# Kernel optimization log

Hardware: AMD Instinct MI355X
Metric: run time of the kernel (lower is better)

Reference implementation:

```python
import jax, jax.numpy as jnp
import numpy as np

K_PLG = 9
LN_EPS = 1e-5

def _layer_norm(x, g, b):
    mu = jnp.mean(x, axis=-1, keepdims=True)
    v = jnp.mean((x - mu) ** 2, axis=-1, keepdims=True)
    return (x - mu) / jnp.sqrt(v + LN_EPS) * g + b

def _label_to_patch_agg(label, patch, k):
    # squared euclidean distances (S, N); sqrt is monotonic so top-k indices
    # match torch.cdist(p=2).topk(largest=False)
    d2 = (jnp.sum(label * label, axis=1)[:, None]
          + jnp.sum(patch * patch, axis=1)[None, :]
          - 2.0 * label @ patch.T)
    _, idx = jax.lax.top_k(-d2, k)          # (S, k) nearest
    nbr = patch[idx]                         # (S, k, C)
    return jnp.max(nbr - label[:, None, :], axis=1)  # max-relative diff (S, C)

def setup_inputs() -> dict:
    key = jax.random.key(0)
    ks = jax.random.split(key, 12)
    N, C = 100000, 256
    n_mood, n_genre, n_sub = 64, 256, 1024
    s = 1.0 / np.sqrt(C)
    return {
        "patch_emb": jax.random.normal(ks[0], (N, C), jnp.float32),
        "mood_emb": jax.random.normal(ks[1], (n_mood, C), jnp.float32),
        "genre_emb": jax.random.normal(ks[2], (n_genre, C), jnp.float32),
        "sub_emb": jax.random.normal(ks[3], (n_sub, C), jnp.float32),
        "Wm": jax.random.normal(ks[4], (2 * C, C), jnp.float32) * s,
        "bm": jnp.zeros((C,), jnp.float32),
        "Wg": jax.random.normal(ks[5], (3 * C, C), jnp.float32) * s,
        "bg": jnp.zeros((C,), jnp.float32),
        "Ws": jax.random.normal(ks[6], (4 * C, C), jnp.float32) * s,
        "bs": jnp.zeros((C,), jnp.float32),
        "gm": jnp.ones((C,), jnp.float32), "bnm": jnp.zeros((C,), jnp.float32),
        "gg": jnp.ones((C,), jnp.float32), "bng": jnp.zeros((C,), jnp.float32),
        "gs": jnp.ones((C,), jnp.float32), "bns": jnp.zeros((C,), jnp.float32),
    }

def reference(patch_emb, mood_emb, genre_emb, sub_emb,
              Wm, bm, Wg, bg, Ws, bs, gm, bnm, gg, bng, gs, bns):
    k = K_PLG
    # mood level
    ctx_m = _label_to_patch_agg(mood_emb, patch_emb, k)
    mood = _layer_norm(
        mood_emb + jnp.concatenate([mood_emb, ctx_m], axis=-1) @ Wm + bm, gm, bnm)
    # genre level
    ctx_g_p = _label_to_patch_agg(genre_emb, patch_emb, k)
    ctx_g_m = _label_to_patch_agg(genre_emb, mood, max(1, k // 2))
    genre = _layer_norm(
        genre_emb + jnp.concatenate([genre_emb, ctx_g_p, ctx_g_m], axis=-1) @ Wg + bg,
        gg, bng)
    # sub-genre level
    ctx_s_p = _label_to_patch_agg(sub_emb, patch_emb, k)
    ctx_s_m = _label_to_patch_agg(sub_emb, mood, max(1, k // 3))
    ctx_s_g = _label_to_patch_agg(sub_emb, genre, max(1, k // 2))
    sub = _layer_norm(
        sub_emb + jnp.concatenate([sub_emb, ctx_s_p, ctx_s_m, ctx_s_g], axis=-1) @ Ws + bs,
        gs, bns)
    return (mood, genre, sub)
```

## Files before the change

### kernel.cpp

```cpp
#include <hip/hip_runtime.h>
#include <float.h>

#define N_PATCH 100000
#define C 256
#define S_TOT 1344
#define LBLK 32
#define NGRP 42
#define NCHUNK 24
#define CHUNKP 4224
#define NTILE 1563
#define KCC 10
#define NCAND (NCHUNK*KCC)
#define NSEL 24
#define KP 9
#define SMASK 0xFFFFE000u
#define KINIT 0x7F7FFFFFu

typedef __attribute__((ext_vector_type(4))) float f32x4;
typedef __attribute__((ext_vector_type(2))) long i64x2;
typedef __attribute__((ext_vector_type(4))) unsigned int u32x4;

static __device__ __forceinline__ unsigned int pk4_fp8(float a, float b, float c, float d) {
  int v = __builtin_amdgcn_cvt_pk_fp8_f32(a, b, 0, false);
  v = __builtin_amdgcn_cvt_pk_fp8_f32(c, d, v, true);
  return (unsigned int)v;
}

#define KNET3(K0, K1, K2, KV)                               \
  { unsigned int _kv = (KV);                                \
    K2 = min(K2, max(K1, _kv));                             \
    K1 = min(K1, max(K0, _kv));                             \
    K0 = min(K0, _kv); }

__global__ __launch_bounds__(256) void k_prep(
    const float* __restrict__ patch, const float* __restrict__ me,
    const float* __restrict__ ge, const float* __restrict__ se,
    unsigned char* __restrict__ patchT, unsigned char* __restrict__ lblQ,
    float* __restrict__ hp2) {
  int bid = blockIdx.x;
  int t = threadIdx.x;
  if (bid < NTILE) {
    const int T = bid;
    {
      int r = t >> 2, i = t & 3;
      int row = min(T * 64 + r, N_PATCH - 1);
      const float4* src = reinterpret_cast<const float4*>(patch + (size_t)row * C);
      float s = 0.f;
      #pragma unroll
      for (int u = 0; u < 16; ++u) {
        float4 v = src[i + 4 * u];
        s += v.x*v.x + v.y*v.y + v.z*v.z + v.w*v.w;
      }
      s += __shfl_xor(s, 1, 64);
      s += __shfl_xor(s, 2, 64);
      if (i == 0 && T * 64 + r < N_PATCH) hp2[T * 64 + r] = 0.5f * s + 512.0f;
    }
    #pragma unroll
    for (int u = 0; u < 4; ++u) {
      int q = (t >> 6) & 3, l = t & 63;
      int rr = u * 16 + (l & 15), g = l >> 4;
      int prow = min(T * 64 + rr, N_PATCH - 1);
      const float* pr = patch + (size_t)prow * C;
      int k0 = 64 * q + 8 * g;
      float4 aa = *reinterpret_cast<const float4*>(pr + k0);
      float4 bb = *reinterpret_cast<const float4*>(pr + k0 + 4);
      float4 cc = *reinterpret_cast<const float4*>(pr + k0 + 32);
      float4 dd = *reinterpret_cast<const float4*>(pr + k0 + 36);
      u32x4 o;
      o.x = pk4_fp8(-aa.x, -aa.y, -aa.z, -aa.w);
      o.y = pk4_fp8(-bb.x, -bb.y, -bb.z, -bb.w);
      o.z = pk4_fp8(-cc.x, -cc.y, -cc.z, -cc.w);
      o.w = pk4_fp8(-dd.x, -dd.y, -dd.z, -dd.w);
      *reinterpret_cast<u32x4*>(patchT + ((size_t)T << 14) + (size_t)(u * 256 + t) * 16) = o;
    }
  } else {
    int row = (bid - NTILE) * 4 + (t >> 6);
    int l = t & 63;
    int k0 = 32 * ((l >> 1) & 7) + 8 * (l >> 4) + (l & 1) * 4;
    const float* src = (row < 64) ? me + (size_t)row * C
                     : (row < 320) ? ge + (size_t)(row - 64) * C
                                   : se + (size_t)(row - 320) * C;
    float4 v = *reinterpret_cast<const float4*>(src + k0);
    *reinterpret_cast<unsigned int*>(lblQ + (size_t)row * 256 + l * 4) =
        pk4_fp8(v.x, v.y, v.z, v.w);
  }
}

__global__ __launch_bounds__(256, 4) void k_score_mfma(
    const unsigned char* __restrict__ patchT, const unsigned char* __restrict__ lblQ,
    const float* __restrict__ hp2,
    float* __restrict__ candS, int* __restrict__ candI) {
  __shared__ unsigned int ksmem[LBLK * 48];

  const int j = blockIdx.x;
  const int chunk = (j & 7) * 3 + (j >> 3) / NGRP;
  const int grp = (j >> 3) % NGRP;
  const int row0 = grp * LBLK;
  const int p_begin = chunk * CHUNKP;
  const int p_end = min(p_begin + CHUNKP, N_PATCH);
  const int tid = threadIdx.x;
  const int l = tid & 63, w = tid >> 6;
  const int g = l >> 4, r16 = l & 15;

  long bf0[8], bf1[8];
  {
    const unsigned char* b0 = lblQ + ((size_t)(row0 + r16) << 8) + (g << 6);
    #pragma unroll
    for (int q = 0; q < 4; ++q) {
      i64x2 v0 = *reinterpret_cast<const i64x2*>(b0 + q * 16);
      i64x2 v1 = *reinterpret_cast<const i64x2*>(b0 + 4096 + q * 16);
      bf0[2*q] = v0.x; bf0[2*q+1] = v0.y;
      bf1[2*q] = v1.x; bf1[2*q+1] = v1.y;
    }
  }

  unsigned int a0k = KINIT, a1k = KINIT, a2k = KINIT;
  unsigned int b0k = KINIT, b1k = KINIT, b2k = KINIT;

  const int nsteps = (p_end - p_begin + 63) >> 6;
  const int gtile0 = p_begin >> 6;
  const unsigned char* pbase = patchT + ((size_t)gtile0 << 14) + (w << 12) + (l << 4);
  const int hsub = w * 16 + 4 * g;

  i64x2 A0[4], A1[4];
  float4 h0, h1;

  auto loadA = [&](int t, i64x2 (&A)[4]) {
    const unsigned char* p = pbase + ((size_t)t << 14);
    #pragma unroll
    for (int q = 0; q < 4; ++q) A[q] = *reinterpret_cast<const i64x2*>(p + (q << 10));
  };
  auto loadH = [&](int t) -> float4 {
    int hi = p_begin + t * 64 + hsub;
    if (hi > N_PATCH - 4) hi = N_PATCH - 4;
    return *reinterpret_cast<const float4*>(hp2 + hi);
  };

  auto compute = [&](i64x2 (&A)[4], float4 h, int t) {
    f32x4 acc0 = {h.x, h.y, h.z, h.w};
    f32x4 acc1 = acc0;
    __builtin_amdgcn_s_setprio(1);
    #pragma unroll
    for (int q = 0; q < 4; ++q) {
      acc0 = __builtin_amdgcn_mfma_f32_16x16x32_fp8_fp8(A[q].x, bf0[2*q],   acc0, 0, 0, 0);
      acc1 = __builtin_amdgcn_mfma_f32_16x16x32_fp8_fp8(A[q].x, bf1[2*q],   acc1, 0, 0, 0);
      acc0 = __builtin_amdgcn_mfma_f32_16x16x32_fp8_fp8(A[q].y, bf0[2*q+1], acc0, 0, 0, 0);
      acc1 = __builtin_amdgcn_mfma_f32_16x16x32_fp8_fp8(A[q].y, bf1[2*q+1], acc1, 0, 0, 0);
    }
    __builtin_amdgcn_s_setprio(0);
    unsigned int lidx = (unsigned int)(t * 64 + hsub);
    unsigned int l1 = lidx | 1u, l2 = lidx | 2u, l3 = lidx | 3u;
    if (p_begin + t * 64 + 64 <= p_end) {
      KNET3(a0k, a1k, a2k, (__float_as_uint(acc0[0]) & SMASK) | lidx);
      KNET3(a0k, a1k, a2k, (__float_as_uint(acc0[1]) & SMASK) | l1);
      KNET3(a0k, a1k, a2k, (__float_as_uint(acc0[2]) & SMASK) | l2);
      KNET3(a0k, a1k, a2k, (__float_as_uint(acc0[3]) & SMASK) | l3);
      KNET3(b0k, b1k, b2k, (__float_as_uint(acc1[0]) & SMASK) | lidx);
      KNET3(b0k, b1k, b2k, (__float_as_uint(acc1[1]) & SMASK) | l1);
      KNET3(b0k, b1k, b2k, (__float_as_uint(acc1[2]) & SMASK) | l2);
      KNET3(b0k, b1k, b2k, (__float_as_uint(acc1[3]) & SMASK) | l3);
    } else {
      const int pg0 = p_begin + t * 64 + hsub;
      unsigned int k0 = (pg0     < p_end) ? ((__float_as_uint(acc0[0]) & SMASK) | lidx) : KINIT;
      unsigned int k1 = (pg0 + 1 < p_end) ? ((__float_as_uint(acc0[1]) & SMASK) | l1) : KINIT;
      unsigned int k2 = (pg0 + 2 < p_end) ? ((__float_as_uint(acc0[2]) & SMASK) | l2) : KINIT;
      unsigned int k3 = (pg0 + 3 < p_end) ? ((__float_as_uint(acc0[3]) & SMASK) | l3) : KINIT;
      unsigned int m0 = (pg0     < p_end) ? ((__float_as_uint(acc1[0]) & SMASK) | lidx) : KINIT;
      unsigned int m1 = (pg0 + 1 < p_end) ? ((__float_as_uint(acc1[1]) & SMASK) | l1) : KINIT;
      unsigned int m2 = (pg0 + 2 < p_end) ? ((__float_as_uint(acc1[2]) & SMASK) | l2) : KINIT;
      unsigned int m3 = (pg0 + 3 < p_end) ? ((__float_as_uint(acc1[3]) & SMASK) | l3) : KINIT;
      KNET3(a0k, a1k, a2k, k0); KNET3(a0k, a1k, a2k, k1);
      KNET3(a0k, a1k, a2k, k2); KNET3(a0k, a1k, a2k, k3);
      KNET3(b0k, b1k, b2k, m0); KNET3(b0k, b1k, b2k, m1);
      KNET3(b0k, b1k, b2k, m2); KNET3(b0k, b1k, b2k, m3);
    }
  };

  loadA(0, A0); h0 = loadH(0);
  for (int t = 0; t < nsteps; t += 2) {
    loadA(t + 1, A1); h1 = loadH(t + 1);
    compute(A0, h0, t);
    loadA(t + 2, A0); h0 = loadH(t + 2);
    if (t + 1 < nsteps) compute(A1, h1, t + 1);
  }
  __syncthreads();

  const int sub = (w << 2) + g;
  {
    int base0 = (r16 * 16 + sub) * 3;
    int base1 = ((r16 + 16) * 16 + sub) * 3;
    ksmem[base0 + 0] = a0k; ksmem[base0 + 1] = a1k; ksmem[base0 + 2] = a2k;
    ksmem[base1 + 0] = b0k; ksmem[base1 + 1] = b1k; ksmem[base1 + 2] = b2k;
  }
  __syncthreads();
  if (tid < LBLK) {
    unsigned int fk[KCC];
    #pragma unroll
    for (int jj = 0; jj < KCC; ++jj) fk[jj] = KINIT;
    for (int q = 0; q < 48; ++q) {
      unsigned int v = ksmem[tid * 48 + q];
      if (v < fk[KCC-1]) {
        fk[KCC-1] = v;
        #pragma unroll
        for (int qq = KCC-1; qq >= 1; --qq) {
          if (fk[qq] < fk[qq-1]) {
            unsigned int tv = fk[qq]; fk[qq] = fk[qq-1]; fk[qq-1] = tv;
          }
        }
      }
    }
    size_t o = ((size_t)(row0 + tid) * NCHUNK + chunk) * KCC;
    #pragma unroll
    for (int jj = 0; jj < KCC; ++jj) {
      candS[o + jj] = __uint_as_float(fk[jj] & SMASK);
      candI[o + jj] = p_begin + (int)(fk[jj] & 0x1FFFu);
    }
  }
}

__global__ __launch_bounds__(256) void k_rescore_ctx(
    const float* __restrict__ patchF,
    const float* __restrict__ me, const float* __restrict__ ge,
    const float* __restrict__ se,
    const float* __restrict__ hp2, const float* __restrict__ candS,
    const int* __restrict__ candI,
    float* __restrict__ ctx_m, float* __restrict__ ctx_gp, float* __restrict__ ctx_sp) {
  __shared__ float lrow[C];
  __shared__ float ss[NCAND];
  __shared__ int si[NCAND];
  __shared__ int selIdx[NSEL];
  __shared__ float s2[NSEL];
  __shared__ int top[KP];
  int row = blockIdx.x, t = threadIdx.x;
  const float* lsrc = (row < 64) ? me + (size_t)row * C
                    : (row < 320) ? ge + (size_t)(row - 64) * C
                                  : se + (size_t)(row - 320) * C;
  lrow[t] = lsrc[t];
  if (t < NCAND) {
    ss[t] = candS[(size_t)row * NCAND + t];
    si[t] = candI[(size_t)row * NCAND + t];
  }
  __syncthreads();
  if (t < NCAND) {
    float s = ss[t]; int id = si[t];
    int rank = 0;
    for (int q = 0; q < NCAND; ++q) {
      float v = ss[q];
      rank += (v < s) || (v == s && si[q] < id);
    }
    if (rank < NSEL) selIdx[rank] = id;
  }
  __syncthreads();
  {
    int c = t >> 3, l8 = t & 7;
    if (c < NSEL) {
      const float4* pr = reinterpret_cast<const float4*>(patchF + (size_t)selIdx[c] * C);
      const float4* lr = reinterpret_cast<const float4*>(lrow);
      float dx = 0.f, dy = 0.f, dz = 0.f, dw = 0.f;
      #pragma unroll
      for (int i = 0; i < 8; ++i) {
        float4 a = pr[l8 + 8*i], b = lr[l8 + 8*i];
        dx = fmaf(a.x, b.x, dx); dy = fmaf(a.y, b.y, dy);
        dz = fmaf(a.z, b.z, dz); dw = fmaf(a.w, b.w, dw);
      }
      float d = (dx + dy) + (dz + dw);
      #pragma unroll
      for (int off = 1; off < 8; off <<= 1) d += __shfl_xor(d, off, 64);
      if (l8 == 0) s2[c] = hp2[selIdx[c]] - d;
    }
  }
  __syncthreads();
  if (t == 0) {
    float fs[KP]; int fi[KP];
    #pragma unroll
    for (int jj = 0; jj < KP; ++jj) { fs[jj] = FLT_MAX; fi[jj] = 0; }
    for (int q = 0; q < NSEL; ++q) {
      float v = s2[q];
      if (v < fs[KP-1]) {
        fs[KP-1] = v; fi[KP-1] = selIdx[q];
        #pragma unroll
        for (int qq = KP-1; qq >= 1; --qq) {
          if (fs[qq] < fs[qq-1]) {
            float ts = fs[qq]; fs[qq] = fs[qq-1]; fs[qq-1] = ts;
            int ti = fi[qq]; fi[qq] = fi[qq-1]; fi[qq-1] = ti;
          }
        }
      }
    }
    #pragma unroll
    for (int jj = 0; jj < KP; ++jj) top[jj] = fi[jj];
  }
  __syncthreads();
  float m = -FLT_MAX;
  #pragma unroll
  for (int jj = 0; jj < KP; ++jj)
    m = fmaxf(m, patchF[(size_t)top[jj] * C + t]);
  float* dst; int rr;
  if (row < 64)       { dst = ctx_m;  rr = row; }
  else if (row < 320) { dst = ctx_gp; rr = row - 64; }
  else                { dst = ctx_sp; rr = row - 320; }
  dst[(size_t)rr * C + t] = m - lrow[t];
}

template <int R>
__global__ __launch_bounds__(256) void k_out(
    const float* __restrict__ emb, const float* __restrict__ c0,
    const float* __restrict__ c1, const float* __restrict__ c2,
    const float* __restrict__ W, const float* __restrict__ bias,
    const float* __restrict__ gamma, const float* __restrict__ beta,
    float* __restrict__ out, int nin) {
  __shared__ float x[R][1024];
  __shared__ float red[4][R];
  const int row0 = blockIdx.x * R, t = threadIdx.x;
  const int nv = nin >> 2;
  #pragma unroll
  for (int rr = 0; rr < R; ++rr) {
    if (t < nv) {
      int seg = t >> 6;
      const float* src = seg == 0 ? emb : seg == 1 ? c0 : seg == 2 ? c1 : c2;
      *reinterpret_cast<float4*>(&x[rr][t << 2]) =
          *reinterpret_cast<const float4*>(src + (size_t)(row0 + rr) * C + ((t & 63) << 2));
    }
  }
  __syncthreads();
  float acc[R];
  #pragma unroll
  for (int rr = 0; rr < R; ++rr) acc[rr] = 0.f;
  for (int i0 = 0; i0 < nin; i0 += 8) {
    float wv[8];
    #pragma unroll
    for (int u = 0; u < 8; ++u) wv[u] = W[(size_t)(i0 + u) * C + t];
    #pragma unroll
    for (int u = 0; u < 8; ++u) {
      #pragma unroll
      for (int rr = 0; rr < R; ++rr) acc[rr] = fmaf(x[rr][i0 + u], wv[u], acc[rr]);
    }
  }
  float bv = bias[t];
  float y[R], d[R];
  int wv_ = t >> 6, ln = t & 63;
  #pragma unroll
  for (int rr = 0; rr < R; ++rr) {
    y[rr] = x[rr][t] + acc[rr] + bv;
    float sum = y[rr];
    #pragma unroll
    for (int off = 32; off; off >>= 1) sum += __shfl_down(sum, off, 64);
    if (ln == 0) red[wv_][rr] = sum;
  }
  __syncthreads();
  float mu[R];
  #pragma unroll
  for (int rr = 0; rr < R; ++rr)
    mu[rr] = (red[0][rr] + red[1][rr] + red[2][rr] + red[3][rr]) * (1.f / C);
  __syncthreads();
  #pragma unroll
  for (int rr = 0; rr < R; ++rr) {
    d[rr] = y[rr] - mu[rr];
    float sq = d[rr] * d[rr];
    #pragma unroll
    for (int off = 32; off; off >>= 1) sq += __shfl_down(sq, off, 64);
    if (ln == 0) red[wv_][rr] = sq;
  }
  __syncthreads();
  #pragma unroll
  for (int rr = 0; rr < R; ++rr) {
    float var = (red[0][rr] + red[1][rr] + red[2][rr] + red[3][rr]) * (1.f / C);
    out[(size_t)(row0 + rr) * C + t] = d[rr] * rsqrtf(var + 1e-5f) * gamma[t] + beta[t];
  }
}

__global__ __launch_bounds__(512) void k_out_g(
    const float* __restrict__ genre_e, const float* __restrict__ ctx_gp,
    const float* __restrict__ out_m,
    const float* __restrict__ W, const float* __restrict__ bias,
    const float* __restrict__ gamma, const float* __restrict__ beta,
    float* __restrict__ out) {
  __shared__ float x[2][1024];
  __shared__ float ds[2][64];
  __shared__ int sel[2][4];
  __shared__ float red[8];
  const int row0 = blockIdx.x * 2, t = threadIdx.x;
  const int w = t >> 6, ln = t & 63;
  if (t < 256) {
    int rr = t >> 7, seg = (t >> 6) & 1, c4 = (t & 63) << 2;
    const float* src = seg ? ctx_gp : genre_e;
    *reinterpret_cast<float4*>(&x[rr][seg * 256 + c4]) =
        *reinterpret_cast<const float4*>(src + (size_t)(row0 + rr) * C + c4);
  }
  __syncthreads();
  {
    int q = t & 3, pr = t >> 2;
    int rr = pr >> 6, ri = pr & 63;
    const float4* rp = reinterpret_cast<const float4*>(out_m + (size_t)ri * C);
    const float4* qp = reinterpret_cast<const float4*>(x[rr]);
    float s = 0.f;
    #pragma unroll
    for (int i = 0; i < 16; ++i) {
      float4 a = rp[i * 4 + q];
      float4 b = qp[i * 4 + q];
      float e;
      e = a.x - b.x; s = fmaf(e, e, s); e = a.y - b.y; s = fmaf(e, e, s);
      e = a.z - b.z; s = fmaf(e, e, s); e = a.w - b.w; s = fmaf(e, e, s);
    }
    s += __shfl_xor(s, 1, 64);
    s += __shfl_xor(s, 2, 64);
    if (q == 0) ds[rr][ri] = s;
  }
  __syncthreads();
  if (w < 2) {
    for (int jj = 0; jj < 4; ++jj) {
      float m = ds[w][ln]; int mi_ = ln;
      #pragma unroll
      for (int off = 32; off; off >>= 1) {
        float om = __shfl_down(m, off, 64);
        int oi = __shfl_down(mi_, off, 64);
        if (om < m) { m = om; mi_ = oi; }
      }
      mi_ = __shfl(mi_, 0, 64);
      if (ln == 0) sel[w][jj] = mi_;
      ds[w][mi_] = FLT_MAX;
    }
  }
  __syncthreads();
  {
    int rr = t >> 8, c = t & 255;
    float m = -FLT_MAX;
    #pragma unroll
    for (int jj = 0; jj < 4; ++jj) m = fmaxf(m, out_m[(size_t)sel[rr][jj] * C + c]);
    x[rr][512 + c] = m - x[rr][c];
  }
  __syncthreads();
  const int col = t & 255, rg = t >> 8;
  float acc = 0.f;
  const float* xr = x[rg];
  for (int i0 = 0; i0 < 768; i0 += 16) {
    float wv[16];
    #pragma unroll
    for (int u = 0; u < 16; ++u) wv[u] = W[(size_t)(i0 + u) * C + col];
    #pragma unroll
    for (int u = 0; u < 16; ++u) acc = fmaf(xr[i0 + u], wv[u], acc);
  }
  float y = xr[col] + acc + bias[col];
  {
    float sum = y;
    #pragma unroll
    for (int off = 32; off; off >>= 1) sum += __shfl_down(sum, off, 64);
    if (ln == 0) red[w] = sum;
  }
  __syncthreads();
  int wb = rg * 4;
  float mu = (red[wb] + red[wb+1] + red[wb+2] + red[wb+3]) * (1.f / C);
  __syncthreads();
  float d = y - mu;
  {
    float sq = d * d;
    #pragma unroll
    for (int off = 32; off; off >>= 1) sq += __shfl_down(sq, off, 64);
    if (ln == 0) red[w] = sq;
  }
  __syncthreads();
  float var = (red[wb] + red[wb+1] + red[wb+2] + red[wb+3]) * (1.f / C);
  out[(size_t)(row0 + rg) * C + col] = d * rsqrtf(var + 1e-5f) * gamma[col] + beta[col];
}

__global__ __launch_bounds__(512) void k_out_s(
    const float* __restrict__ sub_e, const float* __restrict__ ctx_sp,
    const float* __restrict__ out_m, const float* __restrict__ out_g,
    const float* __restrict__ W, const float* __restrict__ bias,
    const float* __restrict__ gamma, const float* __restrict__ beta,
    float* __restrict__ out) {
  __shared__ float x[4][1024];
  __shared__ float ds[4][256];
  __shared__ int sel[4][4];
  __shared__ float red[8][2];
  const int row0 = blockIdx.x * 4, t = threadIdx.x;
  const int w = t >> 6, ln = t & 63;
  {
    int rr = t >> 7, seg = (t >> 6) & 1, c4 = (t & 63) << 2;
    const float* src = seg ? ctx_sp : sub_e;
    *reinterpret_cast<float4*>(&x[rr][seg * 256 + c4]) =
        *reinterpret_cast<const float4*>(src + (size_t)(row0 + rr) * C + c4);
  }
  __syncthreads();
  #pragma unroll
  for (int u = 0; u < 2; ++u) {
    int unit = u * 512 + t;
    int q = unit & 3, pr = unit >> 2;
    int rr = pr >> 6, ri = pr & 63;
    const float4* rp = reinterpret_cast<const float4*>(out_m + (size_t)ri * C);
    const float4* qp = reinterpret_cast<const float4*>(x[rr]);
    float s = 0.f;
    #pragma unroll
    for (int i = 0; i < 16; ++i) {
      float4 a = rp[i * 4 + q];
      float4 b = qp[i * 4 + q];
      float e;
      e = a.x - b.x; s = fmaf(e, e, s); e = a.y - b.y; s = fmaf(e, e, s);
      e = a.z - b.z; s = fmaf(e, e, s); e = a.w - b.w; s = fmaf(e, e, s);
    }
    s += __shfl_xor(s, 1, 64);
    s += __shfl_xor(s, 2, 64);
    if (q == 0) ds[rr][ri] = s;
  }
  __syncthreads();
  if (w < 4) {
    for (int jj = 0; jj < 3; ++jj) {
      float m = ds[w][ln]; int mi_ = ln;
      #pragma unroll
      for (int off = 32; off; off >>= 1) {
        float om = __shfl_down(m, off, 64);
        int oi = __shfl_down(mi_, off, 64);
        if (om < m) { m = om; mi_ = oi; }
      }
      mi_ = __shfl(mi_, 0, 64);
      if (ln == 0) sel[w][jj] = mi_;
      ds[w][mi_] = FLT_MAX;
    }
  }
  __syncthreads();
  #pragma unroll
  for (int u = 0; u < 2; ++u) {
    int idx = u * 512 + t;
    int rr = idx >> 8, c = idx & 255;
    float m = -FLT_MAX;
    #pragma unroll
    for (int jj = 0; jj < 3; ++jj) m = fmaxf(m, out_m[(size_t)sel[rr][jj] * C + c]);
    x[rr][512 + c] = m - x[rr][c];
  }
  __syncthreads();
  #pragma unroll
  for (int u = 0; u < 8; ++u) {
    int unit = u * 512 + t;
    int q = unit & 3, pr = unit >> 2;
    int rr = pr >> 8, ri = pr & 255;
    const float4* rp = reinterpret_cast<const float4*>(out_g + (size_t)ri * C);
    const float4* qp = reinterpret_cast<const float4*>(x[rr]);
    float s = 0.f;
    #pragma unroll
    for (int i = 0; i < 16; ++i) {
      float4 a = rp[i * 4 + q];
      float4 b = qp[i * 4 + q];
      float e;
      e = a.x - b.x; s = fmaf(e, e, s); e = a.y - b.y; s = fmaf(e, e, s);
      e = a.z - b.z; s = fmaf(e, e, s); e = a.w - b.w; s = fmaf(e, e, s);
    }
    s += __shfl_xor(s, 1, 64);
    s += __shfl_xor(s, 2, 64);
    if (q == 0) ds[rr][ri] = s;
  }
  __syncthreads();
  if (w < 4) {
    for (int jj = 0; jj < 4; ++jj) {
      float m = ds[w][ln]; int mi_ = ln;
      #pragma unroll
      for (int o = 64; o < 256; o += 64) {
        float v = ds[w][ln + o];
        if (v < m) { m = v; mi_ = ln + o; }
      }
      #pragma unroll
      for (int off = 32; off; off >>= 1) {
        float om = __shfl_down(m, off, 64);
        int oi = __shfl_down(mi_, off, 64);
        if (om < m) { m = om; mi_ = oi; }
      }
      mi_ = __shfl(mi_, 0, 64);
      if (ln == 0) sel[w][jj] = mi_;
      ds[w][mi_] = FLT_MAX;
    }
  }
  __syncthreads();
  #pragma unroll
  for (int u = 0; u < 2; ++u) {
    int idx = u * 512 + t;
    int rr = idx >> 8, c = idx & 255;
    float m = -FLT_MAX;
    #pragma unroll
    for (int jj = 0; jj < 4; ++jj) m = fmaxf(m, out_g[(size_t)sel[rr][jj] * C + c]);
    x[rr][768 + c] = m - x[rr][c];
  }
  __syncthreads();
  const int col = t & 255, rg = t >> 8;
  float acc0 = 0.f, acc1 = 0.f;
  const float* xr0 = x[2 * rg];
  const float* xr1 = x[2 * rg + 1];
  for (int i0 = 0; i0 < 1024; i0 += 16) {
    float wv[16];
    #pragma unroll
    for (int u = 0; u < 16; ++u) wv[u] = W[(size_t)(i0 + u) * C + col];
    #pragma unroll
    for (int u = 0; u < 16; ++u) {
      acc0 = fmaf(xr0[i0 + u], wv[u], acc0);
      acc1 = fmaf(xr1[i0 + u], wv[u], acc1);
    }
  }
  float bv = bias[col];
  float y0 = xr0[col] + acc0 + bv;
  float y1 = xr1[col] + acc1 + bv;
  {
    float s0 = y0, s1 = y1;
    #pragma unroll
    for (int off = 32; off; off >>= 1) {
      s0 += __shfl_down(s0, off, 64);
      s1 += __shfl_down(s1, off, 64);
    }
    if (ln == 0) { red[w][0] = s0; red[w][1] = s1; }
  }
  __syncthreads();
  int wb = rg * 4;
  float mu0 = (red[wb][0] + red[wb+1][0] + red[wb+2][0] + red[wb+3][0]) * (1.f / C);
  float mu1 = (red[wb][1] + red[wb+1][1] + red[wb+2][1] + red[wb+3][1]) * (1.f / C);
  __syncthreads();
  float d0 = y0 - mu0, d1 = y1 - mu1;
  {
    float s0 = d0 * d0, s1 = d1 * d1;
    #pragma unroll
    for (int off = 32; off; off >>= 1) {
      s0 += __shfl_down(s0, off, 64);
      s1 += __shfl_down(s1, off, 64);
    }
    if (ln == 0) { red[w][0] = s0; red[w][1] = s1; }
  }
  __syncthreads();
  float v0 = (red[wb][0] + red[wb+1][0] + red[wb+2][0] + red[wb+3][0]) * (1.f / C);
  float v1 = (red[wb][1] + red[wb+1][1] + red[wb+2][1] + red[wb+3][1]) * (1.f / C);
  float gv = gamma[col], bbv = beta[col];
  out[(size_t)(row0 + 2*rg    ) * C + col] = d0 * rsqrtf(v0 + 1e-5f) * gv + bbv;
  out[(size_t)(row0 + 2*rg + 1) * C + col] = d1 * rsqrtf(v1 + 1e-5f) * gv + bbv;
}

extern "C" void kernel_launch(void* const* d_in, const int* in_sizes, int n_in,
                              void* d_out, int out_size, void* d_ws, size_t ws_size,
                              hipStream_t stream) {
  const float* patch   = (const float*)d_in[0];
  const float* mood_e  = (const float*)d_in[1];
  const float* genre_e = (const float*)d_in[2];
  const float* sub_e   = (const float*)d_in[3];
  const float* Wm  = (const float*)d_in[4];
  const float* bm  = (const float*)d_in[5];
  const float* Wg  = (const float*)d_in[6];
  const float* bg  = (const float*)d_in[7];
  const float* Ws  = (const float*)d_in[8];
  const float* bs_ = (const float*)d_in[9];
  const float* gm  = (const float*)d_in[10];
  const float* bnm = (const float*)d_in[11];
  const float* gg  = (const float*)d_in[12];
  const float* bng = (const float*)d_in[13];
  const float* gs  = (const float*)d_in[14];
  const float* bns = (const float*)d_in[15];

  char* ws = (char*)d_ws;
  size_t off = 0;
  auto alloc = [&](size_t bytes) { void* p = ws + off; off = (off + bytes + 255) & ~(size_t)255; return p; };
  unsigned char* patchT = (unsigned char*)alloc((size_t)(NTILE + 2) * 16384);
  unsigned char* lblQ   = (unsigned char*)alloc((size_t)S_TOT * 256);
  float* hp2   = (float*)alloc((size_t)N_PATCH * 4);
  float* candS = (float*)alloc((size_t)S_TOT * NCAND * 4);
  int*   candI = (int*)  alloc((size_t)S_TOT * NCAND * 4);
  float* ctx_m  = (float*)alloc((size_t)64   * C * 4);
  float* ctx_gp = (float*)alloc((size_t)256  * C * 4);
  float* ctx_sp = (float*)alloc((size_t)1024 * C * 4);

  float* out_m = (float*)d_out;
  float* out_g = out_m + 64 * C;
  float* out_s = out_g + 256 * C;

  k_prep<<<NTILE + S_TOT / 4, 256, 0, stream>>>(patch, mood_e, genre_e, sub_e,
                                                patchT, lblQ, hp2);
  k_score_mfma<<<NGRP * NCHUNK, 256, 0, stream>>>(patchT, lblQ, hp2, candS, candI);
  k_rescore_ctx<<<S_TOT, 256, 0, stream>>>(patch, mood_e, genre_e, sub_e, hp2,
                                           candS, candI, ctx_m, ctx_gp, ctx_sp);
  k_out<2><<<32, 256, 0, stream>>>(mood_e, ctx_m, nullptr, nullptr, Wm, bm, gm, bnm,
                                   out_m, 512);
  k_out_g<<<128, 512, 0, stream>>>(genre_e, ctx_gp, out_m, Wg, bg, gg, bng, out_g);
  k_out_s<<<256, 512, 0, stream>>>(sub_e, ctx_sp, out_m, out_g, Ws, bs_, gs, bns, out_s);
}
```

Baseline: 205.9 us.

## Stage patch tiles through LDS, fuse mood output into rescore, split-K output GEMVs

k_prep now reads each patch row once, coalesced, into a swizzled LDS tile and computes the norms from it, then builds the fp8 transposed tile from LDS instead of reissuing strided global loads. The mood-level linear plus layernorm is folded into k_rescore_ctx for the first 64 rows, which removes the k_out launch. k_out_g and k_out_s now split the K dimension across the two 256-thread halves, so each W element is loaded once per block, and the partial sums are reduced through LDS. In exchange this uses 64KB of LDS in k_prep, which may reduce occupancy, and adds a serial tail to the mood rescore blocks.

```diff
diff --git a/kernel.cpp b/kernel.cpp
--- a/kernel.cpp
+++ b/kernel.cpp
@@ -37,35 +37,34 @@
     const float* __restrict__ ge, const float* __restrict__ se,
     unsigned char* __restrict__ patchT, unsigned char* __restrict__ lblQ,
     float* __restrict__ hp2) {
+  __shared__ float4 xs[4096];
   int bid = blockIdx.x;
   int t = threadIdx.x;
   if (bid < NTILE) {
     const int T = bid;
-    {
-      int r = t >> 2, i = t & 3;
-      int row = min(T * 64 + r, N_PATCH - 1);
-      const float4* src = reinterpret_cast<const float4*>(patch + (size_t)row * C);
-      float s = 0.f;
-      #pragma unroll
-      for (int u = 0; u < 16; ++u) {
-        float4 v = src[i + 4 * u];
-        s += v.x*v.x + v.y*v.y + v.z*v.z + v.w*v.w;
-      }
-      s += __shfl_xor(s, 1, 64);
-      s += __shfl_xor(s, 2, 64);
-      if (i == 0 && T * 64 + r < N_PATCH) hp2[T * 64 + r] = 0.5f * s + 512.0f;
-    }
+    const int w = t >> 6, l = t & 63;
+    #pragma unroll
+    for (int i = 0; i < 16; ++i) {
+      int row = 4 * i + w;
+      int grow = min(T * 64 + row, N_PATCH - 1);
+      float4 v = reinterpret_cast<const float4*>(patch + (size_t)grow * C)[l];
+      xs[row * 64 + (l ^ (row & 7))] = v;
+      float s = v.x*v.x + v.y*v.y + v.z*v.z + v.w*v.w;
+      #pragma unroll
+      for (int off = 32; off; off >>= 1) s += __shfl_down(s, off, 64);
+      if (l == 0 && T * 64 + row < N_PATCH) hp2[T * 64 + row] = 0.5f * s + 512.0f;
+    }
+    __syncthreads();
+    const int q = (t >> 6) & 3, g = (t >> 4) & 3, r16 = t & 15;
+    const int b4 = 16 * q + 2 * g;
     #pragma unroll
     for (int u = 0; u < 4; ++u) {
-      int q = (t >> 6) & 3, l = t & 63;
-      int rr = u * 16 + (l & 15), g = l >> 4;
-      int prow = min(T * 64 + rr, N_PATCH - 1);
-      const float* pr = patch + (size_t)prow * C;
-      int k0 = 64 * q + 8 * g;
-      float4 aa = *reinterpret_cast<const float4*>(pr + k0);
-      float4 bb = *reinterpret_cast<const float4*>(pr + k0 + 4);
-      float4 cc = *reinterpret_cast<const float4*>(pr + k0 + 32);
-      float4 dd = *reinterpret_cast<const float4*>(pr + k0 + 36);
+      int rr = u * 16 + r16;
+      int xm = rr & 7;
+      float4 aa = xs[rr * 64 + ((b4    ) ^ xm)];
+      float4 bb = xs[rr * 64 + ((b4 + 1) ^ xm)];
+      float4 cc = xs[rr * 64 + ((b4 + 8) ^ xm)];
+      float4 dd = xs[rr * 64 + ((b4 + 9) ^ xm)];
       u32x4 o;
       o.x = pk4_fp8(-aa.x, -aa.y, -aa.z, -aa.w);
       o.y = pk4_fp8(-bb.x, -bb.y, -bb.z, -bb.w);
@@ -224,13 +223,18 @@
     const float* __restrict__ se,
     const float* __restrict__ hp2, const float* __restrict__ candS,
     const int* __restrict__ candI,
-    float* __restrict__ ctx_m, float* __restrict__ ctx_gp, float* __restrict__ ctx_sp) {
+    float* __restrict__ ctx_m, float* __restrict__ ctx_gp, float* __restrict__ ctx_sp,
+    const float* __restrict__ Wm, const float* __restrict__ bm,
+    const float* __restrict__ gm, const float* __restrict__ bnm,
+    float* __restrict__ out_m) {
   __shared__ float lrow[C];
+  __shared__ float crow[C];
   __shared__ float ss[NCAND];
   __shared__ int si[NCAND];
   __shared__ int selIdx[NSEL];
   __shared__ float s2[NSEL];
   __shared__ int top[KP];
+  __shared__ float red2[4];
   int row = blockIdx.x, t = threadIdx.x;
   const float* lsrc = (row < 64) ? me + (size_t)row * C
                     : (row < 320) ? ge + (size_t)(row - 64) * C
@@ -295,77 +299,47 @@
   #pragma unroll
   for (int jj = 0; jj < KP; ++jj)
     m = fmaxf(m, patchF[(size_t)top[jj] * C + t]);
+  float ctxv = m - lrow[t];
   float* dst; int rr;
   if (row < 64)       { dst = ctx_m;  rr = row; }
   else if (row < 320) { dst = ctx_gp; rr = row - 64; }
   else                { dst = ctx_sp; rr = row - 320; }
-  dst[(size_t)rr * C + t] = m - lrow[t];
-}
-
-template <int R>
-__global__ __launch_bounds__(256) void k_out(
-    const float* __restrict__ emb, const float* __restrict__ c0,
-    const float* __restrict__ c1, const float* __restrict__ c2,
-    const float* __restrict__ W, const float* __restrict__ bias,
-    const float* __restrict__ gamma, const float* __restrict__ beta,
-    float* __restrict__ out, int nin) {
-  __shared__ float x[R][1024];
-  __shared__ float red[4][R];
-  const int row0 = blockIdx.x * R, t = threadIdx.x;
-  const int nv = nin >> 2;
-  #pragma unroll
-  for (int rr = 0; rr < R; ++rr) {
-    if (t < nv) {
-      int seg = t >> 6;
-      const float* src = seg == 0 ? emb : seg == 1 ? c0 : seg == 2 ? c1 : c2;
-      *reinterpret_cast<float4*>(&x[rr][t << 2]) =
-          *reinterpret_cast<const float4*>(src + (size_t)(row0 + rr) * C + ((t & 63) << 2));
-    }
-  }
-  __syncthreads();
-  float acc[R];
-  #pragma unroll
-  for (int rr = 0; rr < R; ++rr) acc[rr] = 0.f;
-  for (int i0 = 0; i0 < nin; i0 += 8) {
-    float wv[8];
-    #pragma unroll
-    for (int u = 0; u < 8; ++u) wv[u] = W[(size_t)(i0 + u) * C + t];
-    #pragma unroll
-    for (int u = 0; u < 8; ++u) {
-      #pragma unroll
-      for (int rr = 0; rr < R; ++rr) acc[rr] = fmaf(x[rr][i0 + u], wv[u], acc[rr]);
-    }
-  }
-  float bv = bias[t];
-  float y[R], d[R];
-  int wv_ = t >> 6, ln = t & 63;
-  #pragma unroll
-  for (int rr = 0; rr < R; ++rr) {
-    y[rr] = x[rr][t] + acc[rr] + bv;
-    float sum = y[rr];
+  dst[(size_t)rr * C + t] = ctxv;
+  if (row < 64) {
+    crow[t] = ctxv;
+    __syncthreads();
+    float acc = 0.f;
+    for (int i0 = 0; i0 < 256; i0 += 16) {
+      float wv[16];
+      #pragma unroll
+      for (int u = 0; u < 16; ++u) wv[u] = Wm[(size_t)(i0 + u) * C + t];
+      #pragma unroll
+      for (int u = 0; u < 16; ++u) acc = fmaf(lrow[i0 + u], wv[u], acc);
+    }
+    for (int i0 = 0; i0 < 256; i0 += 16) {
+      float wv[16];
+      #pragma unroll
+      for (int u = 0; u < 16; ++u) wv[u] = Wm[(size_t)(256 + i0 + u) * C + t];
+      #pragma unroll
+      for (int u = 0; u < 16; ++u) acc = fmaf(crow[i0 + u], wv[u], acc);
+    }
+    float y = lrow[t] + acc + bm[t];
+    int w = t >> 6, ln = t & 63;
+    float sum = y;
     #pragma unroll
     for (int off = 32; off; off >>= 1) sum += __shfl_down(sum, off, 64);
-    if (ln == 0) red[wv_][rr] = sum;
-  }
-  __syncthreads();
-  float mu[R];
-  #pragma unroll
-  for (int rr = 0; rr < R; ++rr)
-    mu[rr] = (red[0][rr] + red[1][rr] + red[2][rr] + red[3][rr]) * (1.f / C);
-  __syncthreads();
-  #pragma unroll
-  for (int rr = 0; rr < R; ++rr) {
-    d[rr] = y[rr] - mu[rr];
-    float sq = d[rr] * d[rr];
+    if (ln == 0) red2[w] = sum;
+    __syncthreads();
+    float mu = (red2[0] + red2[1] + red2[2] + red2[3]) * (1.f / C);
+    __syncthreads();
+    float d = y - mu;
+    float sq = d * d;
     #pragma unroll
     for (int off = 32; off; off >>= 1) sq += __shfl_down(sq, off, 64);
-    if (ln == 0) red[wv_][rr] = sq;
-  }
-  __syncthreads();
-  #pragma unroll
-  for (int rr = 0; rr < R; ++rr) {
-    float var = (red[0][rr] + red[1][rr] + red[2][rr] + red[3][rr]) * (1.f / C);
-    out[(size_t)(row0 + rr) * C + t] = d[rr] * rsqrtf(var + 1e-5f) * gamma[t] + beta[t];
+    if (ln == 0) red2[w] = sq;
+    __syncthreads();
+    float var = (red2[0] + red2[1] + red2[2] + red2[3]) * (1.f / C);
+    out_m[(size_t)row * C + t] = d * rsqrtf(var + 1e-5f) * gm[t] + bnm[t];
   }
 }
 
@@ -378,7 +352,8 @@
   __shared__ float x[2][1024];
   __shared__ float ds[2][64];
   __shared__ int sel[2][4];
-  __shared__ float red[8];
+  __shared__ float part[2][2][256];
+  __shared__ float red[4][2];
   const int row0 = blockIdx.x * 2, t = threadIdx.x;
   const int w = t >> 6, ln = t & 63;
   if (t < 256) {
@@ -430,37 +405,50 @@
     x[rr][512 + c] = m - x[rr][c];
   }
   __syncthreads();
-  const int col = t & 255, rg = t >> 8;
-  float acc = 0.f;
-  const float* xr = x[rg];
-  for (int i0 = 0; i0 < 768; i0 += 16) {
+  const int kg = t >> 8, col = t & 255, base = kg * 384;
+  float a0 = 0.f, a1 = 0.f;
+  for (int i0 = 0; i0 < 384; i0 += 16) {
     float wv[16];
     #pragma unroll
-    for (int u = 0; u < 16; ++u) wv[u] = W[(size_t)(i0 + u) * C + col];
-    #pragma unroll
-    for (int u = 0; u < 16; ++u) acc = fmaf(xr[i0 + u], wv[u], acc);
-  }
-  float y = xr[col] + acc + bias[col];
-  {
-    float sum = y;
-    #pragma unroll
-    for (int off = 32; off; off >>= 1) sum += __shfl_down(sum, off, 64);
-    if (ln == 0) red[w] = sum;
-  }
-  __syncthreads();
-  int wb = rg * 4;
-  float mu = (red[wb] + red[wb+1] + red[wb+2] + red[wb+3]) * (1.f / C);
-  __syncthreads();
-  float d = y - mu;
-  {
-    float sq = d * d;
-    #pragma unroll
-    for (int off = 32; off; off >>= 1) sq += __shfl_down(sq, off, 64);
-    if (ln == 0) red[w] = sq;
-  }
-  __syncthreads();
-  float var = (red[wb] + red[wb+1] + red[wb+2] + red[wb+3]) * (1.f / C);
-  out[(size_t)(row0 + rg) * C + col] = d * rsqrtf(var + 1e-5f) * gamma[col] + beta[col];
+    for (int u = 0; u < 16; ++u) wv[u] = W[(size_t)(base + i0 + u) * C + col];
+    #pragma unroll
+    for (int u = 0; u < 16; ++u) {
+      a0 = fmaf(x[0][base + i0 + u], wv[u], a0);
+      a1 = fmaf(x[1][base + i0 + u], wv[u], a1);
+    }
+  }
+  part[kg][0][col] = a0; part[kg][1][col] = a1;
+  __syncthreads();
+  if (t < 256) {
+    float bv = bias[t];
+    float y0 = x[0][t] + part[0][0][t] + part[1][0][t] + bv;
+    float y1 = x[1][t] + part[0][1][t] + part[1][1][t] + bv;
+    float s0 = y0, s1 = y1;
+    #pragma unroll
+    for (int off = 32; off; off >>= 1) {
+      s0 += __shfl_down(s0, off, 64);
+      s1 += __shfl_down(s1, off, 64);
+    }
+    if (ln == 0) { red[w][0] = s0; red[w][1] = s1; }
+    __syncthreads();
+    float mu0 = (red[0][0] + red[1][0] + red[2][0] + red[3][0]) * (1.f / C);
+    float mu1 = (red[0][1] + red[1][1] + red[2][1] + red[3][1]) * (1.f / C);
+    __syncthreads();
+    float d0 = y0 - mu0, d1 = y1 - mu1;
+    s0 = d0 * d0; s1 = d1 * d1;
+    #pragma unroll
+    for (int off = 32; off; off >>= 1) {
+      s0 += __shfl_down(s0, off, 64);
+      s1 += __shfl_down(s1, off, 64);
+    }
+    if (ln == 0) { red[w][0] = s0; red[w][1] = s1; }
+    __syncthreads();
+    float v0 = (red[0][0] + red[1][0] + red[2][0] + red[3][0]) * (1.f / C);
+    float v1 = (red[0][1] + red[1][1] + red[2][1] + red[3][1]) * (1.f / C);
+    float gv = gamma[t], bbv = beta[t];
+    out[(size_t)(row0    ) * C + t] = d0 * rsqrtf(v0 + 1e-5f) * gv + bbv;
+    out[(size_t)(row0 + 1) * C + t] = d1 * rsqrtf(v1 + 1e-5f) * gv + bbv;
+  }
 }
 
 __global__ __launch_bounds__(512) void k_out_s(
@@ -472,7 +460,8 @@
   __shared__ float x[4][1024];
   __shared__ float ds[4][256];
   __shared__ int sel[4][4];
-  __shared__ float red[8][2];
+  __shared__ float part[2][4][256];
+  __shared__ float red[4][4];
   const int row0 = blockIdx.x * 4, t = threadIdx.x;
   const int w = t >> 6, ln = t & 63;
   {
@@ -579,53 +568,53 @@
     x[rr][768 + c] = m - x[rr][c];
   }
   __syncthreads();
-  const int col = t & 255, rg = t >> 8;
-  float acc0 = 0.f, acc1 = 0.f;
-  const float* xr0 = x[2 * rg];
-  const float* xr1 = x[2 * rg + 1];
-  for (int i0 = 0; i0 < 1024; i0 += 16) {
+  const int kg = t >> 8, col = t & 255, base = kg * 512;
+  float acc[4] = {0.f, 0.f, 0.f, 0.f};
+  for (int i0 = 0; i0 < 512; i0 += 16) {
     float wv[16];
     #pragma unroll
-    for (int u = 0; u < 16; ++u) wv[u] = W[(size_t)(i0 + u) * C + col];
+    for (int u = 0; u < 16; ++u) wv[u] = W[(size_t)(base + i0 + u) * C + col];
     #pragma unroll
     for (int u = 0; u < 16; ++u) {
-      acc0 = fmaf(xr0[i0 + u], wv[u], acc0);
-      acc1 = fmaf(xr1[i0 + u], wv[u], acc1);
-    }
-  }
-  float bv = bias[col];
-  float y0 = xr0[col] + acc0 + bv;
-  float y1 = xr1[col] + acc1 + bv;
-  {
-    float s0 = y0, s1 = y1;
-    #pragma unroll
-    for (int off = 32; off; off >>= 1) {
-      s0 += __shfl_down(s0, off, 64);
-      s1 += __shfl_down(s1, off, 64);
-    }
-    if (ln == 0) { red[w][0] = s0; red[w][1] = s1; }
-  }
-  __syncthreads();
-  int wb = rg * 4;
-  float mu0 = (red[wb][0] + red[wb+1][0] + red[wb+2][0] + red[wb+3][0]) * (1.f / C);
-  float mu1 = (red[wb][1] + red[wb+1][1] + red[wb+2][1] + red[wb+3][1]) * (1.f / C);
-  __syncthreads();
-  float d0 = y0 - mu0, d1 = y1 - mu1;
-  {
-    float s0 = d0 * d0, s1 = d1 * d1;
-    #pragma unroll
-    for (int off = 32; off; off >>= 1) {
-      s0 += __shfl_down(s0, off, 64);
-      s1 += __shfl_down(s1, off, 64);
-    }
-    if (ln == 0) { red[w][0] = s0; red[w][1] = s1; }
-  }
-  __syncthreads();
-  float v0 = (red[wb][0] + red[wb+1][0] + red[wb+2][0] + red[wb+3][0]) * (1.f / C);
-  float v1 = (red[wb][1] + red[wb+1][1] + red[wb+2][1] + red[wb+3][1]) * (1.f / C);
-  float gv = gamma[col], bbv = beta[col];
-  out[(size_t)(row0 + 2*rg    ) * C + col] = d0 * rsqrtf(v0 + 1e-5f) * gv + bbv;
-  out[(size_t)(row0 + 2*rg + 1) * C + col] = d1 * rsqrtf(v1 + 1e-5f) * gv + bbv;
+      #pragma unroll
+      for (int rr = 0; rr < 4; ++rr) acc[rr] = fmaf(x[rr][base + i0 + u], wv[u], acc[rr]);
+    }
+  }
+  #pragma unroll
+  for (int rr = 0; rr < 4; ++rr) part[kg][rr][col] = acc[rr];
+  __syncthreads();
+  if (t < 256) {
+    float bv = bias[t];
+    float y[4], d[4];
+    #pragma unroll
+    for (int rr = 0; rr < 4; ++rr) {
+      y[rr] = x[rr][t] + part[0][rr][t] + part[1][rr][t] + bv;
+      float sum = y[rr];
+      #pragma unroll
+      for (int off = 32; off; off >>= 1) sum += __shfl_down(sum, off, 64);
+      if (ln == 0) red[w][rr] = sum;
+    }
+    __syncthreads();
+    float mu[4];
+    #pragma unroll
+    for (int rr = 0; rr < 4; ++rr)
+      mu[rr] = (red[0][rr] + red[1][rr] + red[2][rr] + red[3][rr]) * (1.f / C);
+    __syncthreads();
+    #pragma unroll
+    for (int rr = 0; rr < 4; ++rr) {
+      d[rr] = y[rr] - mu[rr];
+      float sq = d[rr] * d[rr];
+      #pragma unroll
+      for (int off = 32; off; off >>= 1) sq += __shfl_down(sq, off, 64);
+      if (ln == 0) red[w][rr] = sq;
+    }
+    __syncthreads();
+    #pragma unroll
+    for (int rr = 0; rr < 4; ++rr) {
+      float var = (red[0][rr] + red[1][rr] + red[2][rr] + red[3][rr]) * (1.f / C);
+      out[(size_t)(row0 + rr) * C + t] = d[rr] * rsqrtf(var + 1e-5f) * gamma[t] + beta[t];
+    }
+  }
 }
 
 extern "C" void kernel_launch(void* const* d_in, const int* in_sizes, int n_in,
@@ -668,9 +657,8 @@
                                                 patchT, lblQ, hp2);
   k_score_mfma<<<NGRP * NCHUNK, 256, 0, stream>>>(patchT, lblQ, hp2, candS, candI);
   k_rescore_ctx<<<S_TOT, 256, 0, stream>>>(patch, mood_e, genre_e, sub_e, hp2,
-                                           candS, candI, ctx_m, ctx_gp, ctx_sp);
-  k_out<2><<<32, 256, 0, stream>>>(mood_e, ctx_m, nullptr, nullptr, Wm, bm, gm, bnm,
-                                   out_m, 512);
+                                           candS, candI, ctx_m, ctx_gp, ctx_sp,
+                                           Wm, bm, gm, bnm, out_m);
   k_out_g<<<128, 512, 0, stream>>>(genre_e, ctx_gp, out_m, Wg, bg, gg, bng, out_g);
   k_out_s<<<256, 512, 0, stream>>>(sub_e, ctx_sp, out_m, out_g, Ws, bs_, gs, bns, out_s);
 }
```

Result: faster. 186.4 us, median of 2 (-9.5%).
